# Kernel tuning notes

Measured on AMD Instinct MI355X. Metric: run time of the kernel, lower is better.

The kernel has to match this reference:

```python
import jax, jax.numpy as jnp
import numpy as np

N_EMBD = 1024
N_HEAD = 16
B, T, T_MEM = 4, 1024, 1024


def setup_inputs() -> dict:
    key = jax.random.key(0)
    ks = jax.random.split(key, 11)
    s = 1.0 / np.sqrt(N_EMBD)
    return {
        "q_in": jax.random.normal(ks[0], (B, T, N_EMBD), jnp.float32),
        "k_in": jax.random.normal(ks[1], (B, T_MEM, N_EMBD), jnp.float32),
        "v_in": jax.random.normal(ks[2], (B, T_MEM, N_EMBD), jnp.float32),
        # torch nn.Linear weights: [out_features, in_features]
        "Wq": jax.random.normal(ks[3], (N_EMBD, N_EMBD), jnp.float32) * s,
        "bq": jax.random.normal(ks[4], (N_EMBD,), jnp.float32) * s,
        "Wk": jax.random.normal(ks[5], (N_EMBD, N_EMBD), jnp.float32) * s,
        "bk": jax.random.normal(ks[6], (N_EMBD,), jnp.float32) * s,
        "Wv": jax.random.normal(ks[7], (N_EMBD, N_EMBD), jnp.float32) * s,
        "bv": jax.random.normal(ks[8], (N_EMBD,), jnp.float32) * s,
        "Wo": jax.random.normal(ks[9], (N_EMBD, N_EMBD), jnp.float32) * s,
        "bo": jax.random.normal(ks[10], (N_EMBD,), jnp.float32) * s,
    }


def reference(q_in, k_in, v_in, Wq, bq, Wk, bk, Wv, bv, Wo, bo):
    b, t, c = q_in.shape
    t_mem = k_in.shape[1]
    hd = c // N_HEAD  # head dim

    def proj(x, W, bias):
        return x @ W.T + bias

    # [b, h, t, hd]
    q = proj(q_in, Wq, bq).reshape(b, t, N_HEAD, hd).transpose(0, 2, 1, 3)
    k = proj(k_in, Wk, bk).reshape(b, t_mem, N_HEAD, hd).transpose(0, 2, 1, 3)
    v = proj(v_in, Wv, bv).reshape(b, t_mem, N_HEAD, hd).transpose(0, 2, 1, 3)

    scale = 1.0 / np.sqrt(hd).astype(np.float32)
    att = jnp.einsum("bhqd,bhkd->bhqk", q, k) * scale
    att = jax.nn.softmax(att, axis=-1)  # dropout p=0 -> identity

    y = jnp.einsum("bhqk,bhkd->bhqd", att, v)
    y = y.transpose(0, 2, 1, 3).reshape(b, t, c)
    y = proj(y, Wo, bo)  # resid_drop p=0 -> identity

    attention = jnp.mean(att, axis=1)  # mean over heads: [b, t, t_mem]
    return (y, attention)
```

## Files before the change

kernel.cpp:

```cpp
#include <hip/hip_runtime.h>
#include <hip/hip_fp16.h>


typedef __attribute__((ext_vector_type(8))) short s16x8;
typedef __attribute__((ext_vector_type(4))) float f32x4;
typedef __attribute__((ext_vector_type(4))) unsigned short u16x4;

#define N_EMBD 1024
#define NH 16
#define BT 4096
#define STR 1032

#if __has_builtin(__builtin_amdgcn_global_load_lds)
#define HAVE_GLL 1
#define GLDS16(g, l)                                                              \
  __builtin_amdgcn_global_load_lds((__attribute__((address_space(1))) void*)(g), \
                                   (__attribute__((address_space(3))) void*)(l), 16, 0, 0)
#else
#define HAVE_GLL 0
#endif

static __device__ __forceinline__ unsigned short f2bf(float f) {
  unsigned int u = __builtin_bit_cast(unsigned int, f);
  u += 0x7FFFu + ((u >> 16) & 1u);
  return (unsigned short)(u >> 16);
}
static __device__ __forceinline__ float bf2f(unsigned short h) {
  return __builtin_bit_cast(float, ((unsigned int)h) << 16);
}

__global__ __launch_bounds__(256) void cvt_in3(const float* __restrict__ q,
                                               const float* __restrict__ k,
                                               const float* __restrict__ v,
                                               unsigned short* __restrict__ out) {
  const int z = blockIdx.z;
  const float* src = (z == 0) ? q : (z == 1 ? k : v);
  int i = (blockIdx.x * 256 + threadIdx.x) * 4;
  float4 val = *(const float4*)(src + i);
  u16x4 o;
  o[0] = f2bf(val.x);
  o[1] = f2bf(val.y);
  o[2] = f2bf(val.z);
  o[3] = f2bf(val.w);
  *(u16x4*)(out + (size_t)z * BT * N_EMBD + i) = o;
}

__global__ __launch_bounds__(256) void cvt_w4(const float* __restrict__ wo,
                                              const float* __restrict__ wq,
                                              const float* __restrict__ wk,
                                              const float* __restrict__ wv,
                                              unsigned short* __restrict__ out) {
  const int z = blockIdx.z;
  const float* src = (z == 0) ? wo : (z == 1 ? wq : (z == 2 ? wk : wv));
  const float scale = (z == 1) ? 0.125f : 1.0f;
  int i = (blockIdx.x * 256 + threadIdx.x) * 4;
  float4 val = *(const float4*)(src + i);
  u16x4 o;
  o[0] = f2bf(val.x * scale);
  o[1] = f2bf(val.y * scale);
  o[2] = f2bf(val.z * scale);
  o[3] = f2bf(val.w * scale);
  *(u16x4*)(out + (size_t)z * N_EMBD * N_EMBD + i) = o;
}

template <bool F32OUT>
static __device__ __forceinline__ void gemm_bt_tile(const unsigned short* __restrict__ A,
                                                    const unsigned short* __restrict__ B,
                                                    const float* __restrict__ bias, float bscale,
                                                    void* __restrict__ Cout,
                                                    int m0, int n0, int N, int K,
                                                    unsigned short* Al, unsigned short* Bl) {
  const int tid = threadIdx.x;
  const int l = tid & 63, w = tid >> 6;
  const int wr = w >> 1, wc = w & 1;
  const int l15 = l & 15, l4 = l >> 4;
  const int srow = tid >> 3;
  const int skk = (tid & 7) * 8;
  f32x4 acc[4][4] = {};
  for (int k0 = 0; k0 < K; k0 += 64) {
#if HAVE_GLL
#pragma unroll
    for (int i = 0; i < 4; ++i) {
      GLDS16(&A[(size_t)(m0 + i * 32 + srow) * K + k0 + skk], Al + i * 2048 + w * 512);
      GLDS16(&B[(size_t)(n0 + i * 32 + srow) * K + k0 + skk], Bl + i * 2048 + w * 512);
    }
#else
#pragma unroll
    for (int i = 0; i < 4; ++i) {
      int row = i * 32 + srow;
      *(s16x8*)&Al[row * 64 + skk] = *(const s16x8*)&A[(size_t)(m0 + row) * K + k0 + skk];
      *(s16x8*)&Bl[row * 64 + skk] = *(const s16x8*)&B[(size_t)(n0 + row) * K + k0 + skk];
    }
#endif
    __syncthreads();
#pragma unroll
    for (int kf = 0; kf < 2; ++kf) {
      s16x8 af[4], bfr[4];
#pragma unroll
      for (int mi = 0; mi < 4; ++mi)
        af[mi] = *(const s16x8*)&Al[(wr * 64 + mi * 16 + l15) * 64 + kf * 32 + l4 * 8];
#pragma unroll
      for (int nj = 0; nj < 4; ++nj)
        bfr[nj] = *(const s16x8*)&Bl[(wc * 64 + nj * 16 + l15) * 64 + kf * 32 + l4 * 8];
#pragma unroll
      for (int mi = 0; mi < 4; ++mi) {
#pragma unroll
        for (int nj = 0; nj < 4; ++nj)
          acc[mi][nj] =
              __builtin_amdgcn_mfma_f32_16x16x32_bf16(af[mi], bfr[nj], acc[mi][nj], 0, 0, 0);
      }
    }
    __syncthreads();
  }
#pragma unroll
  for (int nj = 0; nj < 4; ++nj) {
    int col = n0 + wc * 64 + nj * 16 + l15;
    float bv = bias[col] * bscale;
#pragma unroll
    for (int mi = 0; mi < 4; ++mi) {
#pragma unroll
      for (int r = 0; r < 4; ++r) {
        int row = m0 + wr * 64 + mi * 16 + l4 * 4 + r;
        float v = acc[mi][nj][r] + bv;
        if constexpr (F32OUT)
          ((float*)Cout)[(size_t)row * N + col] = v;
        else
          ((unsigned short*)Cout)[(size_t)row * N + col] = f2bf(v);
      }
    }
  }
}

__global__ __launch_bounds__(256) void gemm_qkv(const unsigned short* __restrict__ Xin,
                                                const unsigned short* __restrict__ Wbf,
                                                const float* __restrict__ bq,
                                                const float* __restrict__ bk,
                                                const float* __restrict__ bv,
                                                unsigned short* __restrict__ Cout) {
  __shared__ unsigned short Al[128 * 64];
  __shared__ unsigned short Bl[128 * 64];
  const int z = blockIdx.z;
  const float* bias = (z == 0) ? bq : (z == 1 ? bk : bv);
  const float bscale = (z == 0) ? 0.125f : 1.0f;
  gemm_bt_tile<false>(Xin + (size_t)z * BT * N_EMBD,
                      Wbf + (size_t)(1 + z) * N_EMBD * N_EMBD, bias, bscale,
                      Cout + (size_t)z * BT * N_EMBD, blockIdx.x * 128, blockIdx.y * 128,
                      N_EMBD, N_EMBD, Al, Bl);
}

__global__ __launch_bounds__(256) void gemm_out(const unsigned short* __restrict__ Ybf,
                                                const unsigned short* __restrict__ Wo,
                                                const float* __restrict__ bo,
                                                float* __restrict__ Cout) {
  __shared__ unsigned short Al[128 * 64];
  __shared__ unsigned short Bl[128 * 64];
  gemm_bt_tile<true>(Ybf, Wo, bo, 1.0f, Cout, blockIdx.x * 128, blockIdx.y * 128, N_EMBD, N_EMBD,
                     Al, Bl);
}

__global__ __launch_bounds__(256) void transpose_v(const unsigned short* __restrict__ Vp,
                                                   unsigned short* __restrict__ Vt) {
  __shared__ unsigned short tile[64][65];
  const int t0 = blockIdx.x * 64, h = blockIdx.y, b = blockIdx.z;
  const int r = threadIdx.x >> 2, c0 = (threadIdx.x & 3) * 16;
  const unsigned short* src = Vp + (size_t)(b * 1024 + t0 + r) * 1024 + h * 64 + c0;
#pragma unroll
  for (int j = 0; j < 16; ++j) tile[r][c0 + j] = src[j];
  __syncthreads();
  unsigned short* dst = Vt + (size_t)((b * 16 + h) * 64 + r) * 1024 + t0 + c0;
#pragma unroll
  for (int j = 0; j < 16; ++j) dst[j] = tile[c0 + j][r];
}

__global__ __launch_bounds__(1024, 4) void attn_ph2(const unsigned short* __restrict__ Qp,
                                                    const unsigned short* __restrict__ Kp,
                                                    const unsigned short* __restrict__ Vt,
                                                    unsigned short* __restrict__ Ybf,
                                                    unsigned short* __restrict__ Pmean) {
  __shared__ __align__(16) unsigned short S2[2][32 * STR];
  __shared__ float RedM[2][32][8];
  __shared__ float RedS[2][32][8];
  const int tid = threadIdx.x;
  const int tm = tid >> 9;
  const int ttid = tid & 511;
  const int w4 = ttid >> 6;
  const int l = tid & 63;
  const int l15 = l & 15, l4 = l >> 4;
  const int r = ttid & 31, c = ttid >> 5;
  const int qgw = w4 >> 2;
  const int dtw = w4 & 3;

  const int bid = blockIdx.x;
  const int grp = bid & 7, qt = bid >> 3;
  const int b = grp >> 1, hg = grp & 1;
  const int q0 = qt * 32;

  __half2 am[32];
#pragma unroll
  for (int j = 0; j < 32; ++j) am[j] = __float2half2_rn(0.f);

#pragma unroll 1
  for (int it = 0; it < 4; ++it) {
    const int h = hg * 8 + it * 2 + tm;
    const unsigned short* qb0 = Qp + (size_t)(b * 1024 + q0 + l15) * 1024 + h * 64 + l4 * 8;
    const unsigned short* qb1 = qb0 + (size_t)16 * 1024;
    s16x8 aq00 = *(const s16x8*)qb0;
    s16x8 aq01 = *(const s16x8*)(qb0 + 32);
    s16x8 aq10 = *(const s16x8*)qb1;
    s16x8 aq11 = *(const s16x8*)(qb1 + 32);
    float m0 = -3.4e38f, m1 = -3.4e38f;
#pragma unroll
    for (int nt = 0; nt < 8; ++nt) {
      int gn = w4 * 8 + nt;
      const unsigned short* kb = Kp + (size_t)(b * 1024 + gn * 16 + l15) * 1024 + h * 64 + l4 * 8;
      s16x8 kf0 = *(const s16x8*)kb;
      s16x8 kf1 = *(const s16x8*)(kb + 32);
      f32x4 s0 = {}, s1 = {};
      s0 = __builtin_amdgcn_mfma_f32_16x16x32_bf16(kf0, aq00, s0, 0, 0, 0);
      s0 = __builtin_amdgcn_mfma_f32_16x16x32_bf16(kf1, aq01, s0, 0, 0, 0);
      s1 = __builtin_amdgcn_mfma_f32_16x16x32_bf16(kf0, aq10, s1, 0, 0, 0);
      s1 = __builtin_amdgcn_mfma_f32_16x16x32_bf16(kf1, aq11, s1, 0, 0, 0);
      u16x4 p0, p1;
#pragma unroll
      for (int rr = 0; rr < 4; ++rr) {
        m0 = fmaxf(m0, s0[rr]);
        p0[rr] = f2bf(s0[rr]);
        m1 = fmaxf(m1, s1[rr]);
        p1[rr] = f2bf(s1[rr]);
      }
      *(u16x4*)&S2[tm][l15 * STR + gn * 16 + l4 * 4] = p0;
      *(u16x4*)&S2[tm][(16 + l15) * STR + gn * 16 + l4 * 4] = p1;
    }
    m0 = fmaxf(m0, __shfl_xor(m0, 16));
    m0 = fmaxf(m0, __shfl_xor(m0, 32));
    m1 = fmaxf(m1, __shfl_xor(m1, 16));
    m1 = fmaxf(m1, __shfl_xor(m1, 32));
    if (l < 16) {
      RedM[tm][l][w4] = m0;
      RedM[tm][16 + l][w4] = m1;
    }
    __syncthreads();

    float mm = RedM[tm][r][0];
#pragma unroll
    for (int j = 1; j < 8; ++j) mm = fmaxf(mm, RedM[tm][r][j]);
    float ps = 0.f;
#pragma unroll
    for (int k = 0; k < 8; ++k) {
      unsigned short* sp = &S2[tm][r * STR + c * 64 + k * 8];
      s16x8 sv = *(const s16x8*)sp;
      s16x8 pv;
#pragma unroll
      for (int j = 0; j < 8; ++j) {
        float e = __expf(bf2f((unsigned short)sv[j]) - mm);
        ps += e;
        pv[j] = (short)f2bf(e);
      }
      *(s16x8*)sp = pv;
    }
    ps += __shfl_xor(ps, 32);
    if (l < 32) RedS[tm][l][w4] = ps;
    __syncthreads();

    float lsA = 0.f;
#pragma unroll
    for (int j = 0; j < 8; ++j) lsA += RedS[tm][qgw * 16 + l15][j];
    float fac = 0.0625f / lsA;
    f32x4 y = {};
    const unsigned short* vb =
        Vt + (size_t)((b * 16 + h) * 64 + dtw * 16 + l15) * 1024 + l4 * 8;
#pragma unroll
    for (int kq = 0; kq < 4; ++kq) {
#pragma unroll
      for (int kk = 0; kk < 8; ++kk) {
        const int ks = kq * 8 + kk;
        s16x8 pa = *(const s16x8*)&S2[tm][(qgw * 16 + l15) * STR + ks * 32 + l4 * 8];
        y = __builtin_amdgcn_mfma_f32_16x16x32_bf16(pa, *(const s16x8*)(vb + ks * 32), y, 0, 0, 0);
        if (kq == dtw) {
#pragma unroll
          for (int e2 = 0; e2 < 4; ++e2) {
            float2 fv;
            fv.x = bf2f((unsigned short)pa[e2 * 2]) * fac;
            fv.y = bf2f((unsigned short)pa[e2 * 2 + 1]) * fac;
            am[kk * 4 + e2] = __hadd2(am[kk * 4 + e2], __float22half2_rn(fv));
          }
        }
      }
    }
#pragma unroll
    for (int rr = 0; rr < 4; ++rr) {
      int row = qgw * 16 + l4 * 4 + rr;
      float lsr = 0.f;
#pragma unroll
      for (int j = 0; j < 8; ++j) lsr += RedS[tm][row][j];
      Ybf[(size_t)(b * 1024 + q0 + row) * 1024 + h * 64 + dtw * 16 + l15] = f2bf(y[rr] / lsr);
    }
    __syncthreads();
  }

  unsigned int* us = (unsigned int*)S2;
  if (tm == 1) {
#pragma unroll
    for (int j = 0; j < 32; ++j) us[ttid * 32 + j] = __builtin_bit_cast(unsigned int, am[j]);
  }
  __syncthreads();
  if (tm == 0) {
    unsigned short* pm = Pmean + ((size_t)(b * 2 + hg) << 20) +
                         (size_t)(q0 + qgw * 16 + l15) * 1024 + dtw * 256 + l4 * 8;
#pragma unroll
    for (int kk = 0; kk < 8; ++kk) {
      s16x8 ov;
#pragma unroll
      for (int e2 = 0; e2 < 4; ++e2) {
        int j = kk * 4 + e2;
        __half2 ot = __builtin_bit_cast(__half2, us[ttid * 32 + j]);
        float2 fo = __half22float2(ot);
        float2 fm = __half22float2(am[j]);
        ov[e2 * 2] = (short)f2bf(fm.x + fo.x);
        ov[e2 * 2 + 1] = (short)f2bf(fm.y + fo.y);
      }
      *(s16x8*)&pm[kk * 32] = ov;
    }
  }
}

__global__ __launch_bounds__(256) void mean2(const unsigned short* __restrict__ P2,
                                             float* __restrict__ out) {
  size_t f = ((size_t)blockIdx.x * 256 + threadIdx.x) * 8;
  int b = (int)(f >> 20);
  size_t i0 = f + ((size_t)b << 20);
  s16x8 a = *(const s16x8*)&P2[i0];
  s16x8 d = *(const s16x8*)&P2[i0 + (1u << 20)];
  float4 o0, o1;
  o0.x = bf2f((unsigned short)a[0]) + bf2f((unsigned short)d[0]);
  o0.y = bf2f((unsigned short)a[1]) + bf2f((unsigned short)d[1]);
  o0.z = bf2f((unsigned short)a[2]) + bf2f((unsigned short)d[2]);
  o0.w = bf2f((unsigned short)a[3]) + bf2f((unsigned short)d[3]);
  o1.x = bf2f((unsigned short)a[4]) + bf2f((unsigned short)d[4]);
  o1.y = bf2f((unsigned short)a[5]) + bf2f((unsigned short)d[5]);
  o1.z = bf2f((unsigned short)a[6]) + bf2f((unsigned short)d[6]);
  o1.w = bf2f((unsigned short)a[7]) + bf2f((unsigned short)d[7]);
  *(float4*)&out[f] = o0;
  *(float4*)&out[f + 4] = o1;
}

extern "C" void kernel_launch(void* const* d_in, const int* in_sizes, int n_in, void* d_out,
                              int out_size, void* d_ws, size_t ws_size, hipStream_t stream) {
  const float* q_in = (const float*)d_in[0];
  const float* k_in = (const float*)d_in[1];
  const float* v_in = (const float*)d_in[2];
  const float* Wq = (const float*)d_in[3];
  const float* bq = (const float*)d_in[4];
  const float* Wk = (const float*)d_in[5];
  const float* bk = (const float*)d_in[6];
  const float* Wv = (const float*)d_in[7];
  const float* bv = (const float*)d_in[8];
  const float* Wo = (const float*)d_in[9];
  const float* bo = (const float*)d_in[10];

  float* out_y = (float*)d_out;
  float* out_att = out_y + (size_t)BT * N_EMBD;

  char* ws = (char*)d_ws;
  const size_t MB = 1024 * 1024;
  unsigned short* xin_bf = (unsigned short*)(ws);
  unsigned short* W_bf = (unsigned short*)(ws + 24 * MB);
  unsigned short* Qp = (unsigned short*)(ws + 32 * MB);
  unsigned short* Kp = Qp + (size_t)BT * N_EMBD;
  unsigned short* Vp = Kp + (size_t)BT * N_EMBD;
  unsigned short* Pmean = (unsigned short*)(ws);
  unsigned short* Vt = (unsigned short*)(ws + 16 * MB);
  unsigned short* Ybf = Vp;

  const int NIN = BT * N_EMBD;
  const int NW = N_EMBD * N_EMBD;

  cvt_in3<<<dim3(NIN / 1024, 1, 3), 256, 0, stream>>>(q_in, k_in, v_in, xin_bf);
  cvt_w4<<<dim3(NW / 1024, 1, 4), 256, 0, stream>>>(Wo, Wq, Wk, Wv, W_bf);

  gemm_qkv<<<dim3(BT / 128, N_EMBD / 128, 3), 256, 0, stream>>>(xin_bf, W_bf, bq, bk, bv, Qp);
  transpose_v<<<dim3(16, 16, 4), 256, 0, stream>>>(Vp, Vt);
  attn_ph2<<<256, 1024, 0, stream>>>(Qp, Kp, Vt, Ybf, Pmean);
  mean2<<<2048, 256, 0, stream>>>(Pmean, out_att);
  gemm_out<<<dim3(BT / 128, N_EMBD / 128), 256, 0, stream>>>(Ybf, W_bf, bo, out_y);
}
```

Baseline: 222.2 us.

## Use per-wave local softmax max to drop a barrier in attention

Each wave now exponentiates its own score columns right after the QK MFMAs, using its wave-local row max, and publishes (max, sum) pairs. This removes one block-wide barrier and a separate pass that re-read the score tile from shared memory. The PV accumulation is split into 8 per-segment accumulators, which are rescaled by exp(local max - global max) at the end, and the head-mean probabilities are scaled the same way. Packed bf16 conversion and s_setprio around the MFMA loops are also added. In exchange it uses more registers for the 8 accumulators and does extra exp work, and the per-segment max makes rounding differ slightly from the old version.

```diff
diff --git a/kernel.cpp b/kernel.cpp
--- a/kernel.cpp
+++ b/kernel.cpp
@@ -27,6 +27,11 @@
 }
 static __device__ __forceinline__ float bf2f(unsigned short h) {
   return __builtin_bit_cast(float, ((unsigned int)h) << 16);
+}
+static __device__ __forceinline__ unsigned int pk_bf16(float lo, float hi) {
+  unsigned int r;
+  asm("v_cvt_pk_bf16_f32 %0, %1, %2" : "=v"(r) : "v"(lo), "v"(hi));
+  return r;
 }
 
 __global__ __launch_bounds__(256) void cvt_in3(const float* __restrict__ q,
@@ -178,15 +183,13 @@
                                                     unsigned short* __restrict__ Ybf,
                                                     unsigned short* __restrict__ Pmean) {
   __shared__ __align__(16) unsigned short S2[2][32 * STR];
-  __shared__ float RedM[2][32][8];
-  __shared__ float RedS[2][32][8];
+  __shared__ float2 RedSM[2][32][8];
   const int tid = threadIdx.x;
   const int tm = tid >> 9;
   const int ttid = tid & 511;
   const int w4 = ttid >> 6;
   const int l = tid & 63;
   const int l15 = l & 15, l4 = l >> 4;
-  const int r = ttid & 31, c = ttid >> 5;
   const int qgw = w4 >> 2;
   const int dtw = w4 & 3;
 
@@ -209,6 +212,7 @@
     s16x8 aq10 = *(const s16x8*)qb1;
     s16x8 aq11 = *(const s16x8*)(qb1 + 32);
     float m0 = -3.4e38f, m1 = -3.4e38f;
+    __builtin_amdgcn_s_setprio(1);
 #pragma unroll
     for (int nt = 0; nt < 8; ++nt) {
       int gn = w4 * 8 + nt;
@@ -231,52 +235,75 @@
       *(u16x4*)&S2[tm][l15 * STR + gn * 16 + l4 * 4] = p0;
       *(u16x4*)&S2[tm][(16 + l15) * STR + gn * 16 + l4 * 4] = p1;
     }
+    __builtin_amdgcn_s_setprio(0);
     m0 = fmaxf(m0, __shfl_xor(m0, 16));
     m0 = fmaxf(m0, __shfl_xor(m0, 32));
     m1 = fmaxf(m1, __shfl_xor(m1, 16));
     m1 = fmaxf(m1, __shfl_xor(m1, 32));
+
+    float ps0 = 0.f, ps1 = 0.f;
+#pragma unroll
+    for (int nt = 0; nt < 8; ++nt) {
+      int gn = w4 * 8 + nt;
+      unsigned short* sp0 = &S2[tm][l15 * STR + gn * 16 + l4 * 4];
+      unsigned short* sp1 = &S2[tm][(16 + l15) * STR + gn * 16 + l4 * 4];
+      u16x4 r0 = *(const u16x4*)sp0;
+      u16x4 r1 = *(const u16x4*)sp1;
+      float e00 = __expf(bf2f(r0[0]) - m0);
+      float e01 = __expf(bf2f(r0[1]) - m0);
+      float e02 = __expf(bf2f(r0[2]) - m0);
+      float e03 = __expf(bf2f(r0[3]) - m0);
+      float e10 = __expf(bf2f(r1[0]) - m1);
+      float e11 = __expf(bf2f(r1[1]) - m1);
+      float e12 = __expf(bf2f(r1[2]) - m1);
+      float e13 = __expf(bf2f(r1[3]) - m1);
+      ps0 += (e00 + e01) + (e02 + e03);
+      ps1 += (e10 + e11) + (e12 + e13);
+      uint2 k0, k1;
+      k0.x = pk_bf16(e00, e01);
+      k0.y = pk_bf16(e02, e03);
+      k1.x = pk_bf16(e10, e11);
+      k1.y = pk_bf16(e12, e13);
+      *(uint2*)sp0 = k0;
+      *(uint2*)sp1 = k1;
+    }
+    ps0 += __shfl_xor(ps0, 16);
+    ps0 += __shfl_xor(ps0, 32);
+    ps1 += __shfl_xor(ps1, 16);
+    ps1 += __shfl_xor(ps1, 32);
     if (l < 16) {
-      RedM[tm][l][w4] = m0;
-      RedM[tm][16 + l][w4] = m1;
+      RedSM[tm][l][w4] = make_float2(m0, ps0);
+      RedSM[tm][16 + l][w4] = make_float2(m1, ps1);
     }
     __syncthreads();
 
-    float mm = RedM[tm][r][0];
-#pragma unroll
-    for (int j = 1; j < 8; ++j) mm = fmaxf(mm, RedM[tm][r][j]);
-    float ps = 0.f;
-#pragma unroll
-    for (int k = 0; k < 8; ++k) {
-      unsigned short* sp = &S2[tm][r * STR + c * 64 + k * 8];
-      s16x8 sv = *(const s16x8*)sp;
-      s16x8 pv;
-#pragma unroll
-      for (int j = 0; j < 8; ++j) {
-        float e = __expf(bf2f((unsigned short)sv[j]) - mm);
-        ps += e;
-        pv[j] = (short)f2bf(e);
-      }
-      *(s16x8*)sp = pv;
-    }
-    ps += __shfl_xor(ps, 32);
-    if (l < 32) RedS[tm][l][w4] = ps;
-    __syncthreads();
-
-    float lsA = 0.f;
-#pragma unroll
-    for (int j = 0; j < 8; ++j) lsA += RedS[tm][qgw * 16 + l15][j];
-    float fac = 0.0625f / lsA;
-    f32x4 y = {};
+    float Mq = RedSM[tm][qgw * 16 + l15][0].x;
+#pragma unroll
+    for (int j = 1; j < 8; ++j) Mq = fmaxf(Mq, RedSM[tm][qgw * 16 + l15][j].x);
+    float Lq = 0.f;
+#pragma unroll
+    for (int j = 0; j < 8; ++j) {
+      float2 v = RedSM[tm][qgw * 16 + l15][j];
+      Lq += v.y * __expf(v.x - Mq);
+    }
+    const float sA = __expf(RedSM[tm][qgw * 16 + l15][dtw * 2].x - Mq) / Lq * 0.0625f;
+    const float sB = __expf(RedSM[tm][qgw * 16 + l15][dtw * 2 + 1].x - Mq) / Lq * 0.0625f;
+
+    f32x4 ys[8] = {};
     const unsigned short* vb =
         Vt + (size_t)((b * 16 + h) * 64 + dtw * 16 + l15) * 1024 + l4 * 8;
+    __builtin_amdgcn_s_setprio(1);
 #pragma unroll
     for (int kq = 0; kq < 4; ++kq) {
 #pragma unroll
       for (int kk = 0; kk < 8; ++kk) {
         const int ks = kq * 8 + kk;
+        const int seg = kq * 2 + (kk >> 2);
         s16x8 pa = *(const s16x8*)&S2[tm][(qgw * 16 + l15) * STR + ks * 32 + l4 * 8];
-        y = __builtin_amdgcn_mfma_f32_16x16x32_bf16(pa, *(const s16x8*)(vb + ks * 32), y, 0, 0, 0);
+        ys[seg] =
+            __builtin_amdgcn_mfma_f32_16x16x32_bf16(pa, *(const s16x8*)(vb + ks * 32), ys[seg], 0, 0, 0);
         if (kq == dtw) {
+          const float fac = (kk < 4) ? sA : sB;
 #pragma unroll
           for (int e2 = 0; e2 < 4; ++e2) {
             float2 fv;
@@ -287,13 +314,22 @@
         }
       }
     }
+    __builtin_amdgcn_s_setprio(0);
 #pragma unroll
     for (int rr = 0; rr < 4; ++rr) {
-      int row = qgw * 16 + l4 * 4 + rr;
-      float lsr = 0.f;
-#pragma unroll
-      for (int j = 0; j < 8; ++j) lsr += RedS[tm][row][j];
-      Ybf[(size_t)(b * 1024 + q0 + row) * 1024 + h * 64 + dtw * 16 + l15] = f2bf(y[rr] / lsr);
+      const int row = qgw * 16 + l4 * 4 + rr;
+      float M = RedSM[tm][row][0].x;
+#pragma unroll
+      for (int j = 1; j < 8; ++j) M = fmaxf(M, RedSM[tm][row][j].x);
+      float L = 0.f, acc = 0.f;
+#pragma unroll
+      for (int j = 0; j < 8; ++j) {
+        float2 v = RedSM[tm][row][j];
+        float sc = __expf(v.x - M);
+        L += v.y * sc;
+        acc += ys[j][rr] * sc;
+      }
+      Ybf[(size_t)(b * 1024 + q0 + row) * 1024 + h * 64 + dtw * 16 + l15] = f2bf(acc / L);
     }
     __syncthreads();
   }
```

Result: no change. 223.2 us (+0.4%).
